# Optimization experiments

Hardware: AMD Instinct MI355X
Metric: run time of the kernel (lower is better)

## Reference

```python
import jax, jax.numpy as jnp
import numpy as np

N, D, E = 65536, 64, 4096


def setup_inputs() -> dict:
    key = jax.random.key(0)
    k1, k2, k3 = jax.random.split(key, 3)
    return {
        "input_data": jax.random.normal(k1, (N, D), dtype=jnp.float32),
        "codebook": jax.random.normal(k2, (E, D), dtype=jnp.float32),
        "dither": jax.random.uniform(k3, (E - 1,), dtype=jnp.float32),
        "entries": E,
    }


def _decode(frac_idx, cb):
    # linear interpolation between consecutive codebook entries
    e = cb.shape[0]
    ii = jnp.clip(jnp.floor(frac_idx), 0, e - 2).astype(jnp.int32)
    r = (frac_idx - ii.astype(frac_idx.dtype))[..., None]
    return (1.0 - r) * cb[ii] + r * cb[ii + 1]


def reference(input_data, codebook, dither, entries):
    cur = codebook[:entries]                                   # (E, D)
    # fractional_index = dither + linspace(0, E-2, E-1) == dither + arange(E-1)
    frac = dither + jnp.arange(entries - 1, dtype=dither.dtype)
    dithered_cb = _decode(frac, cur)                           # (E-1, D)
    # squared euclidean distances via expansion (same argmin as (x-c)^2 sum)
    x2 = jnp.sum(input_data * input_data, axis=1, keepdims=True)   # (N, 1)
    c2 = jnp.sum(dithered_cb * dithered_cb, axis=1)                # (E-1,)
    dist = x2 - 2.0 * (input_data @ dithered_cb.T) + c2[None, :]   # (N, E-1)
    integer_index = jnp.argmin(dist, axis=1)                       # (N,)
    quantized = _decode(integer_index.astype(input_data.dtype), dithered_cb)
    # perplexity = exp(entropy of codebook usage) over `entries` bins
    counts = jnp.zeros((entries,), dtype=jnp.float32).at[integer_index].add(1.0)
    avg_probs = counts / input_data.shape[0]
    perplexity = jnp.exp(-jnp.sum(avg_probs * jnp.log(avg_probs + 1e-10)))
    return quantized, perplexity, integer_index
```

## Files before the change

kernel.cpp:

```cpp
#include <hip/hip_runtime.h>
#include <math.h>


constexpr int D = 64;
constexpr int CHUNK = 64;
constexpr int NTILES = CHUNK / 16;
constexpr int E_PAD = 4096;
constexpr int ESLICES = 2;
constexpr int SLICE = E_PAD / ESLICES;
constexpr int NCH = SLICE / CHUNK;
constexpr float TAU = 0.01f;
constexpr int NSLICE = 8;
constexpr int SLICE_E = E_PAD / NSLICE;
constexpr int BLK = 256;

typedef __attribute__((ext_vector_type(8))) short bf16x8;
typedef __attribute__((ext_vector_type(4))) float f32x4;

__device__ inline unsigned short f2bf(float x) {
  unsigned int u = __float_as_uint(x);
  u = (u + 0x7fffu + ((u >> 16) & 1u)) >> 16;
  return (unsigned short)u;
}
__device__ inline float bf2f(unsigned short h) {
  return __uint_as_float(((unsigned int)h) << 16);
}

__device__ __forceinline__ void gll16(const void* g, void* l) {
  __builtin_amdgcn_global_load_lds(
      (const __attribute__((address_space(1))) unsigned int*)g,
      (__attribute__((address_space(3))) unsigned int*)l, 16, 0, 0);
}
__device__ __forceinline__ void gll4(const void* g, void* l) {
  __builtin_amdgcn_global_load_lds(
      (const __attribute__((address_space(1))) unsigned int*)g,
      (__attribute__((address_space(3))) unsigned int*)l, 4, 0, 0);
}

__global__ __launch_bounds__(256) void build_kernel(
    const float* __restrict__ cb, const float* __restrict__ dither,
    float* __restrict__ dcb, unsigned short* __restrict__ dcbh,
    unsigned short* __restrict__ dcbl, float* __restrict__ c2h,
    float* __restrict__ counts, int* __restrict__ rescue_n, int E, int Em1) {
  int i = blockIdx.x * 4 + (threadIdx.x >> 6);
  int k = threadIdx.x & 63;
  if (k == 0) counts[i] = 0.0f;
  if (i == 0 && k == 1) *rescue_n = 0;
  if (i >= Em1) {
    dcb[(size_t)i * D + k] = 0.f;
    dcbh[(size_t)i * D + k] = 0;
    dcbl[(size_t)i * D + k] = 0;
    if (k == 0) c2h[i] = 3.0e38f;
    return;
  }
  float frac = dither[i] + (float)i;
  int ii = (int)floorf(frac);
  ii = max(0, min(ii, E - 2));
  float r = frac - (float)ii;
  float v = (1.0f - r) * cb[(size_t)ii * D + k] + r * cb[(size_t)(ii + 1) * D + k];
  dcb[(size_t)i * D + k] = v;
  unsigned short h = f2bf(v);
  unsigned short l = f2bf(v - bf2f(h));
  dcbh[(size_t)i * D + k] = h;
  dcbl[(size_t)i * D + k] = l;
  float s = v * v;
#pragma unroll
  for (int off = 32; off > 0; off >>= 1) s += __shfl_down(s, off, 64);
  if (k == 0) c2h[i] = 0.5f * s;
}

__global__ __launch_bounds__(BLK, 4) void vq_mfma_kernel(
    const float* __restrict__ X, const unsigned short* __restrict__ dcbh,
    const unsigned short* __restrict__ dcbl, const float* __restrict__ c2h,
    float* __restrict__ out_b1, int* __restrict__ out_i1,
    float* __restrict__ out_b2, int N) {
  __shared__ unsigned short s_h[2][CHUNK * D];
  __shared__ unsigned short s_l[2][CHUNK * D];
  __shared__ float s_c2[2][CHUNK];

  const int tid = threadIdx.x;
  const int lane = tid & 63;
  const int wv = tid >> 6;
  const int col = lane & 15;
  const int kg = lane >> 4;
  const int slice = blockIdx.y;
  const int sbase = slice * SLICE;
  const int wvbase = blockIdx.x * 128 + wv * 32;

  bf16x8 ah0[2], ah1[2], al0[2], al1[2];
#pragma unroll
  for (int rg = 0; rg < 2; ++rg) {
    const float* xp = X + (size_t)(wvbase + rg * 16 + col) * D + kg * 8;
#pragma unroll
    for (int i = 0; i < 8; ++i) {
      float x0 = xp[i], x1 = xp[32 + i];
      unsigned short h0 = f2bf(x0), h1 = f2bf(x1);
      ah0[rg][i] = (short)h0; ah1[rg][i] = (short)h1;
      al0[rg][i] = (short)f2bf(x0 - bf2f(h0));
      al1[rg][i] = (short)f2bf(x1 - bf2f(h1));
    }
  }

  float b1[2][4], b2[2][4];
  int i1[2][4];
#pragma unroll
  for (int rg = 0; rg < 2; ++rg)
#pragma unroll
    for (int r = 0; r < 4; ++r) { b1[rg][r] = -3.4e38f; b2[rg][r] = -3.4e38f; i1[rg][r] = sbase; }

  const int xs = col & 7;

  auto stage = [&](int ch, int buf) {
#pragma unroll
    for (int i = 0; i < 2; ++i) {
      const int u = (wv * 2 + i) * 64 + lane;
      const int e = u >> 3, g = u & 7;
      const size_t goff = (((size_t)(sbase + ch * CHUNK + e)) << 6) + ((g ^ (e & 7)) << 3);
      char* dst_h = (char*)s_h[buf] + (size_t)(wv * 2 + i) * 1024;
      char* dst_l = (char*)s_l[buf] + (size_t)(wv * 2 + i) * 1024;
      gll16(dcbh + goff, dst_h);
      gll16(dcbl + goff, dst_l);
    }
    if (wv == 0) {
      gll4(c2h + sbase + ch * CHUNK + lane, (char*)s_c2[buf]);
    }
  };

  stage(0, 0);
  __syncthreads();
  int cur = 0;

  for (int ch = 0; ch < NCH; ++ch) {
    const int ebase = sbase + ch * CHUNK;
    if (ch + 1 < NCH) stage(ch + 1, cur ^ 1);

#pragma unroll
    for (int p = 0; p < 2; ++p) {
      bf16x8 Bh0[2], Bh1[2], Bl0[2], Bl1[2];
      float hc2[2];
#pragma unroll
      for (int q = 0; q < 2; ++q) {
        const int el = (p * 2 + q) * 16 + col;
        const char* bb = (const char*)s_h[cur] + el * 128;
        const char* ll = (const char*)s_l[cur] + el * 128;
        Bh0[q] = *(const bf16x8*)(bb + ((kg ^ xs) << 4));
        Bh1[q] = *(const bf16x8*)(bb + (((kg + 4) ^ xs) << 4));
        Bl0[q] = *(const bf16x8*)(ll + ((kg ^ xs) << 4));
        Bl1[q] = *(const bf16x8*)(ll + (((kg + 4) ^ xs) << 4));
        hc2[q] = s_c2[cur][el];
      }
      f32x4 acc[2][2];
#pragma unroll
      for (int q = 0; q < 2; ++q)
#pragma unroll
        for (int rg = 0; rg < 2; ++rg)
          acc[q][rg] = {-hc2[q], -hc2[q], -hc2[q], -hc2[q]};
      __builtin_amdgcn_s_setprio(1);
#pragma unroll
      for (int q = 0; q < 2; ++q)
#pragma unroll
        for (int rg = 0; rg < 2; ++rg) {
          acc[q][rg] = __builtin_amdgcn_mfma_f32_16x16x32_bf16(ah0[rg], Bh0[q], acc[q][rg], 0, 0, 0);
          acc[q][rg] = __builtin_amdgcn_mfma_f32_16x16x32_bf16(ah1[rg], Bh1[q], acc[q][rg], 0, 0, 0);
          acc[q][rg] = __builtin_amdgcn_mfma_f32_16x16x32_bf16(ah0[rg], Bl0[q], acc[q][rg], 0, 0, 0);
          acc[q][rg] = __builtin_amdgcn_mfma_f32_16x16x32_bf16(ah1[rg], Bl1[q], acc[q][rg], 0, 0, 0);
          acc[q][rg] = __builtin_amdgcn_mfma_f32_16x16x32_bf16(al0[rg], Bh0[q], acc[q][rg], 0, 0, 0);
          acc[q][rg] = __builtin_amdgcn_mfma_f32_16x16x32_bf16(al1[rg], Bh1[q], acc[q][rg], 0, 0, 0);
        }
      __builtin_amdgcn_s_setprio(0);
#pragma unroll
      for (int q = 0; q < 2; ++q) {
        const int colg = ebase + (p * 2 + q) * 16 + col;
#pragma unroll
        for (int rg = 0; rg < 2; ++rg)
#pragma unroll
          for (int r = 0; r < 4; ++r) {
            float s = acc[q][rg][r];
            bool gt = s > b1[rg][r];
            b2[rg][r] = __builtin_amdgcn_fmed3f(b2[rg][r], s, b1[rg][r]);
            b1[rg][r] = fmaxf(b1[rg][r], s);
            i1[rg][r] = gt ? colg : i1[rg][r];
          }
      }
    }

    __syncthreads();
    cur ^= 1;
  }

#pragma unroll
  for (int m = 1; m < 16; m <<= 1) {
#pragma unroll
    for (int rg = 0; rg < 2; ++rg)
#pragma unroll
      for (int r = 0; r < 4; ++r) {
        float ob1 = __shfl_xor(b1[rg][r], m, 64);
        float ob2 = __shfl_xor(b2[rg][r], m, 64);
        int oi1 = __shfl_xor(i1[rg][r], m, 64);
        float loser = fminf(b1[rg][r], ob1);
        b2[rg][r] = fmaxf(fmaxf(b2[rg][r], ob2), loser);
        bool take = (ob1 > b1[rg][r]) || (ob1 == b1[rg][r] && oi1 < i1[rg][r]);
        b1[rg][r] = take ? ob1 : b1[rg][r];
        i1[rg][r] = take ? oi1 : i1[rg][r];
      }
  }
  if (col == 0) {
#pragma unroll
    for (int rg = 0; rg < 2; ++rg)
#pragma unroll
      for (int r = 0; r < 4; ++r) {
        int row = wvbase + rg * 16 + kg * 4 + r;
        size_t o = (size_t)slice * N + row;
        out_b1[o] = b1[rg][r];
        out_i1[o] = i1[rg][r];
        out_b2[o] = b2[rg][r];
      }
  }
}

__global__ __launch_bounds__(64) void finish_kernel(
    const float* __restrict__ out_b1, const int* __restrict__ out_i1,
    const float* __restrict__ out_b2,
    const float* __restrict__ dcb, float* __restrict__ outq,
    float* __restrict__ outidx, float* __restrict__ counts,
    int* __restrict__ rescue_n, int* __restrict__ rescue_list, int N) {
  __shared__ int s_idx[64];
  const int lane = threadIdx.x;
  const int rowbase = blockIdx.x * 64;
  const int row = rowbase + lane;

  float b1c = out_b1[row];
  int bi = out_i1[row];
  float b2c = out_b2[row];
#pragma unroll
  for (int k = 1; k < ESLICES; ++k) {
    float sk = out_b1[(size_t)k * N + row];
    int ek = out_i1[(size_t)k * N + row];
    float qk = out_b2[(size_t)k * N + row];
    b2c = fmaxf(fmaxf(b2c, qk), fminf(sk, b1c));
    bool take = sk > b1c;
    b1c = take ? sk : b1c;
    bi = take ? ek : bi;
  }
  float gap2 = 2.0f * (b1c - b2c);

  outidx[row] = (float)bi;
  s_idx[lane] = bi;
  if (gap2 < TAU) {
    int p = atomicAdd(rescue_n, 1);
    rescue_list[p] = row;
  } else {
    atomicAdd(&counts[bi], 1.0f);
  }
  __syncthreads();

  const float4* dcb4 = (const float4*)dcb;
  float4* outq4 = (float4*)outq;
  const int rl = lane >> 4;
  const int c4 = lane & 15;
#pragma unroll 4
  for (int t = 0; t < 16; ++t) {
    const int rloc = t * 4 + rl;
    const int idx = s_idx[rloc];
    outq4[(size_t)(rowbase + rloc) * 16 + c4] = dcb4[(size_t)idx * 16 + c4];
  }
}

__global__ __launch_bounds__(64) void rescue_scan_kernel(
    const float* __restrict__ X, const float* __restrict__ dcb,
    const float* __restrict__ c2h, const int* __restrict__ rescue_n,
    const int* __restrict__ rescue_list,
    float* __restrict__ pd, int* __restrict__ pi) {
  const int lane = threadIdx.x;
  const int nu = (*rescue_n) * NSLICE;
  for (int u = blockIdx.x; u < nu; u += gridDim.x) {
    const int li = u >> 3;
    const int sl = u & (NSLICE - 1);
    const int row = rescue_list[li];

    const float4* xr = (const float4*)(X + (size_t)row * D);
    float4 x[16];
#pragma unroll
    for (int k = 0; k < 16; ++k) x[k] = xr[k];

    float best = 3.4e38f;
    int bidx = 0x7fffffff;
    const int e0 = sl * SLICE_E;
#pragma unroll 2
    for (int j = 0; j < SLICE_E / 64; ++j) {
      const int e = e0 + j * 64 + lane;
      const float4* cp = (const float4*)(dcb + (size_t)e * D);
      float d0 = 0.f, d1 = 0.f, d2 = 0.f, d3 = 0.f;
#pragma unroll
      for (int k = 0; k < 16; ++k) {
        float4 c = cp[k];
        d0 = fmaf(x[k].x, c.x, d0);
        d1 = fmaf(x[k].y, c.y, d1);
        d2 = fmaf(x[k].z, c.z, d2);
        d3 = fmaf(x[k].w, c.w, d3);
      }
      float d = c2h[e] - ((d0 + d1) + (d2 + d3));
      if (d < best) { best = d; bidx = e; }
    }
#pragma unroll
    for (int m = 1; m < 64; m <<= 1) {
      float od = __shfl_xor(best, m, 64);
      int oi = __shfl_xor(bidx, m, 64);
      if (od < best || (od == best && oi < bidx)) { best = od; bidx = oi; }
    }
    if (lane == 0) { pd[u] = best; pi[u] = bidx; }
  }
}

__global__ __launch_bounds__(64) void rescue_fin_kernel(
    const float* __restrict__ dcb, const int* __restrict__ rescue_n,
    const int* __restrict__ rescue_list, const float* __restrict__ pd,
    const int* __restrict__ pi, float* __restrict__ outq,
    float* __restrict__ outidx, float* __restrict__ counts) {
  const int lane = threadIdx.x;
  const int nr = *rescue_n;
  for (int li = blockIdx.x; li < nr; li += gridDim.x) {
    const int row = rescue_list[li];
    float d = (lane < NSLICE) ? pd[li * NSLICE + lane] : 3.5e38f;
    int ix = (lane < NSLICE) ? pi[li * NSLICE + lane] : 0x7fffffff;
#pragma unroll
    for (int m = 1; m < NSLICE; m <<= 1) {
      float od = __shfl_xor(d, m, 64);
      int oi = __shfl_xor(ix, m, 64);
      if (od < d || (od == d && oi < ix)) { d = od; ix = oi; }
    }
    int bfin = __shfl(ix, 0, 64);
    if (lane == 0) {
      outidx[row] = (float)bfin;
      atomicAdd(&counts[bfin], 1.0f);
    }
    outq[(size_t)row * D + lane] = dcb[(size_t)bfin * D + lane];
  }
}

__global__ __launch_bounds__(256) void vq_perp_kernel(
    const float* __restrict__ counts, float* __restrict__ out, int E, float invN) {
  __shared__ float red[4];
  float s = 0.f;
  for (int j = threadIdx.x; j < E; j += 256) {
    float p = counts[j] * invN;
    s += p * logf(p + 1e-10f);
  }
#pragma unroll
  for (int off = 32; off > 0; off >>= 1) s += __shfl_down(s, off, 64);
  int wid = threadIdx.x >> 6;
  if ((threadIdx.x & 63) == 0) red[wid] = s;
  __syncthreads();
  if (threadIdx.x == 0) {
    float t = (red[0] + red[1]) + (red[2] + red[3]);
    out[0] = expf(-t);
  }
}

static inline size_t align256(size_t x) { return (x + 255) & ~(size_t)255; }

extern "C" void kernel_launch(void* const* d_in, const int* in_sizes, int n_in,
                              void* d_out, int out_size, void* d_ws, size_t ws_size,
                              hipStream_t stream) {
  const float* X      = (const float*)d_in[0];
  const float* cb     = (const float*)d_in[1];
  const float* dither = (const float*)d_in[2];

  const int N   = in_sizes[0] / D;
  const int E   = in_sizes[1] / D;
  const int Em1 = in_sizes[2];

  char* w = (char*)d_ws;
  float* dcb            = (float*)w;          w += align256((size_t)E_PAD * D * sizeof(float));
  unsigned short* dcbh  = (unsigned short*)w; w += align256((size_t)E_PAD * D * sizeof(short));
  unsigned short* dcbl  = (unsigned short*)w; w += align256((size_t)E_PAD * D * sizeof(short));
  float* c2h            = (float*)w;          w += align256((size_t)E_PAD * sizeof(float));
  float* out_b1         = (float*)w;          w += align256((size_t)ESLICES * N * sizeof(float));
  int* out_i1           = (int*)w;            w += align256((size_t)ESLICES * N * sizeof(int));
  float* out_b2         = (float*)w;          w += align256((size_t)ESLICES * N * sizeof(float));
  float* counts         = (float*)w;          w += align256((size_t)E_PAD * sizeof(float));
  int* rescue_n         = (int*)w;            w += align256(sizeof(int));
  int* rescue_list      = (int*)w;            w += align256((size_t)N * sizeof(int));
  float* pd             = (float*)w;          w += align256((size_t)N * NSLICE * sizeof(float));
  int* pi               = (int*)w;            w += align256((size_t)N * NSLICE * sizeof(int));

  float* outq   = (float*)d_out;
  float* perp   = (float*)d_out + (size_t)N * D;
  float* outidx = (float*)d_out + (size_t)N * D + 1;

  build_kernel<<<E_PAD / 4, 256, 0, stream>>>(cb, dither, dcb, dcbh, dcbl, c2h,
                                              counts, rescue_n, E, Em1);

  dim3 g2(N / 128, ESLICES);
  vq_mfma_kernel<<<g2, BLK, 0, stream>>>(X, dcbh, dcbl, c2h, out_b1, out_i1, out_b2, N);

  finish_kernel<<<N / 64, 64, 0, stream>>>(out_b1, out_i1, out_b2, dcb, outq, outidx,
                                           counts, rescue_n, rescue_list, N);

  rescue_scan_kernel<<<2048, 64, 0, stream>>>(X, dcb, c2h, rescue_n, rescue_list, pd, pi);

  rescue_fin_kernel<<<1024, 64, 0, stream>>>(dcb, rescue_n, rescue_list, pd, pi,
                                             outq, outidx, counts);

  vq_perp_kernel<<<1, 256, 0, stream>>>(counts, perp, E, 1.0f / (float)N);
}
```

Before: 165.4 us.

## Split MFMA accumulator chains and fuse rescue scan with finalize kernel

Within the main MFMA loop, each output tile now accumulates into two independent accumulators that are summed before the argmax update. This halves the length of each dependent MFMA chain so more instructions can be in flight. Separately, the two-kernel rescue path (per-slice partial scans followed by a reduction kernel) is merged into one 256-thread-block kernel. That kernel scans all entries for a row, reduces within the block and writes the output directly, removing one launch and the partial-result buffers. The trade-offs are more accumulator registers in the main kernel and less parallelism per rescued row.

```diff
diff --git a/kernel.cpp b/kernel.cpp
--- a/kernel.cpp
+++ b/kernel.cpp
@@ -10,8 +10,6 @@
 constexpr int SLICE = E_PAD / ESLICES;
 constexpr int NCH = SLICE / CHUNK;
 constexpr float TAU = 0.01f;
-constexpr int NSLICE = 8;
-constexpr int SLICE_E = E_PAD / NSLICE;
 constexpr int BLK = 256;
 
 typedef __attribute__((ext_vector_type(8))) short bf16x8;
@@ -149,23 +147,25 @@
         Bl1[q] = *(const bf16x8*)(ll + (((kg + 4) ^ xs) << 4));
         hc2[q] = s_c2[cur][el];
       }
-      f32x4 acc[2][2];
+      f32x4 accA[2][2], accB[2][2];
 #pragma unroll
       for (int q = 0; q < 2; ++q)
 #pragma unroll
-        for (int rg = 0; rg < 2; ++rg)
-          acc[q][rg] = {-hc2[q], -hc2[q], -hc2[q], -hc2[q]};
+        for (int rg = 0; rg < 2; ++rg) {
+          accA[q][rg] = {-hc2[q], -hc2[q], -hc2[q], -hc2[q]};
+          accB[q][rg] = {0.f, 0.f, 0.f, 0.f};
+        }
       __builtin_amdgcn_s_setprio(1);
 #pragma unroll
       for (int q = 0; q < 2; ++q)
 #pragma unroll
         for (int rg = 0; rg < 2; ++rg) {
-          acc[q][rg] = __builtin_amdgcn_mfma_f32_16x16x32_bf16(ah0[rg], Bh0[q], acc[q][rg], 0, 0, 0);
-          acc[q][rg] = __builtin_amdgcn_mfma_f32_16x16x32_bf16(ah1[rg], Bh1[q], acc[q][rg], 0, 0, 0);
-          acc[q][rg] = __builtin_amdgcn_mfma_f32_16x16x32_bf16(ah0[rg], Bl0[q], acc[q][rg], 0, 0, 0);
-          acc[q][rg] = __builtin_amdgcn_mfma_f32_16x16x32_bf16(ah1[rg], Bl1[q], acc[q][rg], 0, 0, 0);
-          acc[q][rg] = __builtin_amdgcn_mfma_f32_16x16x32_bf16(al0[rg], Bh0[q], acc[q][rg], 0, 0, 0);
-          acc[q][rg] = __builtin_amdgcn_mfma_f32_16x16x32_bf16(al1[rg], Bh1[q], acc[q][rg], 0, 0, 0);
+          accA[q][rg] = __builtin_amdgcn_mfma_f32_16x16x32_bf16(ah0[rg], Bh0[q], accA[q][rg], 0, 0, 0);
+          accB[q][rg] = __builtin_amdgcn_mfma_f32_16x16x32_bf16(ah1[rg], Bh1[q], accB[q][rg], 0, 0, 0);
+          accA[q][rg] = __builtin_amdgcn_mfma_f32_16x16x32_bf16(ah0[rg], Bl0[q], accA[q][rg], 0, 0, 0);
+          accB[q][rg] = __builtin_amdgcn_mfma_f32_16x16x32_bf16(ah1[rg], Bl1[q], accB[q][rg], 0, 0, 0);
+          accA[q][rg] = __builtin_amdgcn_mfma_f32_16x16x32_bf16(al0[rg], Bh0[q], accA[q][rg], 0, 0, 0);
+          accB[q][rg] = __builtin_amdgcn_mfma_f32_16x16x32_bf16(al1[rg], Bh1[q], accB[q][rg], 0, 0, 0);
         }
       __builtin_amdgcn_s_setprio(0);
 #pragma unroll
@@ -175,7 +175,7 @@
         for (int rg = 0; rg < 2; ++rg)
 #pragma unroll
           for (int r = 0; r < 4; ++r) {
-            float s = acc[q][rg][r];
+            float s = accA[q][rg][r] + accB[q][rg][r];
             bool gt = s > b1[rg][r];
             b2[rg][r] = __builtin_amdgcn_fmed3f(b2[rg][r], s, b1[rg][r]);
             b1[rg][r] = fmaxf(b1[rg][r], s);
@@ -266,38 +266,35 @@
   }
 }
 
-__global__ __launch_bounds__(64) void rescue_scan_kernel(
+__global__ __launch_bounds__(256) void rescue_kernel(
     const float* __restrict__ X, const float* __restrict__ dcb,
     const float* __restrict__ c2h, const int* __restrict__ rescue_n,
-    const int* __restrict__ rescue_list,
-    float* __restrict__ pd, int* __restrict__ pi) {
-  const int lane = threadIdx.x;
-  const int nu = (*rescue_n) * NSLICE;
-  for (int u = blockIdx.x; u < nu; u += gridDim.x) {
-    const int li = u >> 3;
-    const int sl = u & (NSLICE - 1);
+    const int* __restrict__ rescue_list, float* __restrict__ outq,
+    float* __restrict__ outidx, float* __restrict__ counts, int Em1) {
+  __shared__ float sx[D];
+  __shared__ float sd[4];
+  __shared__ int si[4];
+  __shared__ int sbest;
+  const int tid = threadIdx.x;
+  const int nr = *rescue_n;
+  for (int li = blockIdx.x; li < nr; li += gridDim.x) {
     const int row = rescue_list[li];
-
-    const float4* xr = (const float4*)(X + (size_t)row * D);
-    float4 x[16];
-#pragma unroll
-    for (int k = 0; k < 16; ++k) x[k] = xr[k];
+    __syncthreads();
+    if (tid < D) sx[tid] = X[(size_t)row * D + tid];
+    __syncthreads();
 
     float best = 3.4e38f;
     int bidx = 0x7fffffff;
-    const int e0 = sl * SLICE_E;
-#pragma unroll 2
-    for (int j = 0; j < SLICE_E / 64; ++j) {
-      const int e = e0 + j * 64 + lane;
+    for (int e = tid; e < Em1; e += 256) {
       const float4* cp = (const float4*)(dcb + (size_t)e * D);
       float d0 = 0.f, d1 = 0.f, d2 = 0.f, d3 = 0.f;
 #pragma unroll
       for (int k = 0; k < 16; ++k) {
         float4 c = cp[k];
-        d0 = fmaf(x[k].x, c.x, d0);
-        d1 = fmaf(x[k].y, c.y, d1);
-        d2 = fmaf(x[k].z, c.z, d2);
-        d3 = fmaf(x[k].w, c.w, d3);
+        d0 = fmaf(sx[k * 4 + 0], c.x, d0);
+        d1 = fmaf(sx[k * 4 + 1], c.y, d1);
+        d2 = fmaf(sx[k * 4 + 2], c.z, d2);
+        d3 = fmaf(sx[k * 4 + 3], c.w, d3);
       }
       float d = c2h[e] - ((d0 + d1) + (d2 + d3));
       if (d < best) { best = d; bidx = e; }
@@ -308,33 +305,19 @@
       int oi = __shfl_xor(bidx, m, 64);
       if (od < best || (od == best && oi < bidx)) { best = od; bidx = oi; }
     }
-    if (lane == 0) { pd[u] = best; pi[u] = bidx; }
-  }
-}
-
-__global__ __launch_bounds__(64) void rescue_fin_kernel(
-    const float* __restrict__ dcb, const int* __restrict__ rescue_n,
-    const int* __restrict__ rescue_list, const float* __restrict__ pd,
-    const int* __restrict__ pi, float* __restrict__ outq,
-    float* __restrict__ outidx, float* __restrict__ counts) {
-  const int lane = threadIdx.x;
-  const int nr = *rescue_n;
-  for (int li = blockIdx.x; li < nr; li += gridDim.x) {
-    const int row = rescue_list[li];
-    float d = (lane < NSLICE) ? pd[li * NSLICE + lane] : 3.5e38f;
-    int ix = (lane < NSLICE) ? pi[li * NSLICE + lane] : 0x7fffffff;
-#pragma unroll
-    for (int m = 1; m < NSLICE; m <<= 1) {
-      float od = __shfl_xor(d, m, 64);
-      int oi = __shfl_xor(ix, m, 64);
-      if (od < d || (od == d && oi < ix)) { d = od; ix = oi; }
-    }
-    int bfin = __shfl(ix, 0, 64);
-    if (lane == 0) {
-      outidx[row] = (float)bfin;
-      atomicAdd(&counts[bfin], 1.0f);
-    }
-    outq[(size_t)row * D + lane] = dcb[(size_t)bfin * D + lane];
+    if ((tid & 63) == 0) { sd[tid >> 6] = best; si[tid >> 6] = bidx; }
+    __syncthreads();
+    if (tid == 0) {
+      float bb = sd[0]; int bi2 = si[0];
+      for (int w = 1; w < 4; ++w)
+        if (sd[w] < bb || (sd[w] == bb && si[w] < bi2)) { bb = sd[w]; bi2 = si[w]; }
+      sbest = bi2;
+      outidx[row] = (float)bi2;
+      atomicAdd(&counts[bi2], 1.0f);
+    }
+    __syncthreads();
+    const int bfin = sbest;
+    if (tid < D) outq[(size_t)row * D + tid] = dcb[(size_t)bfin * D + tid];
   }
 }
 
@@ -381,8 +364,6 @@
   float* counts         = (float*)w;          w += align256((size_t)E_PAD * sizeof(float));
   int* rescue_n         = (int*)w;            w += align256(sizeof(int));
   int* rescue_list      = (int*)w;            w += align256((size_t)N * sizeof(int));
-  float* pd             = (float*)w;          w += align256((size_t)N * NSLICE * sizeof(float));
-  int* pi               = (int*)w;            w += align256((size_t)N * NSLICE * sizeof(int));
 
   float* outq   = (float*)d_out;
   float* perp   = (float*)d_out + (size_t)N * D;
@@ -397,10 +378,8 @@
   finish_kernel<<<N / 64, 64, 0, stream>>>(out_b1, out_i1, out_b2, dcb, outq, outidx,
                                            counts, rescue_n, rescue_list, N);
 
-  rescue_scan_kernel<<<2048, 64, 0, stream>>>(X, dcb, c2h, rescue_n, rescue_list, pd, pi);
-
-  rescue_fin_kernel<<<1024, 64, 0, stream>>>(dcb, rescue_n, rescue_list, pd, pi,
-                                             outq, outidx, counts);
+  rescue_kernel<<<2048, 256, 0, stream>>>(X, dcb, c2h, rescue_n, rescue_list,
+                                          outq, outidx, counts, Em1);
 
   vq_perp_kernel<<<1, 256, 0, stream>>>(counts, perp, E, 1.0f / (float)N);
 }
```

Result: slower. 467.7 us (+182.9%).
